# Performance work log

Measured on AMD Instinct MI355X. Metric: run time of the kernel, lower is better.

Reference implementation:

```python
import jax, jax.numpy as jnp
import numpy as np

B, S, D, H = 4, 2048, 1024, 16
HD = D // H

def setup_inputs() -> dict:
    key = jax.random.key(0)
    ks = jax.random.split(key, 11)
    scale = 1.0 / np.sqrt(D)
    return {
        "query": jax.random.normal(ks[0], (B, S, D), jnp.float32),
        "key_": jax.random.normal(ks[1], (B, S, D), jnp.float32),
        "value": jax.random.normal(ks[2], (B, S, D), jnp.float32),
        "wq": jax.random.normal(ks[3], (D, D), jnp.float32) * scale,
        "bq": jnp.zeros((D,), jnp.float32),
        "wk": jax.random.normal(ks[4], (D, D), jnp.float32) * scale,
        "bk": jnp.zeros((D,), jnp.float32),
        "wv": jax.random.normal(ks[5], (D, D), jnp.float32) * scale,
        "bv": jnp.zeros((D,), jnp.float32),
        "wo": jax.random.normal(ks[6], (D, D), jnp.float32) * scale,
        "bo": jnp.zeros((D,), jnp.float32),
    }

def _split_heads(x):
    b, s, _ = x.shape
    return x.reshape(b, s, H, HD).transpose(0, 2, 1, 3)  # [B,H,S,HD]

def reference(query, key_, value, wq, bq, wk, bk, wv, bv, wo, bo):
    q = _split_heads(query @ wq + bq)
    k = _split_heads(key_ @ wk + bk)
    v = _split_heads(value @ wv + bv)
    scores = jnp.einsum('bhqd,bhkd->bhqk', q, k) / jnp.sqrt(jnp.float32(HD))
    attn = jax.nn.softmax(scores, axis=-1)
    ctx = jnp.einsum('bhqk,bhkd->bhqd', attn, v)
    ctx = ctx.transpose(0, 2, 1, 3).reshape(B, S, D)
    return ctx @ wo + bo
```

## Files before the change

kernel.cpp:

```cpp
#include <hip/hip_runtime.h>

typedef _Float16 f16;
typedef _Float16 f16x8 __attribute__((ext_vector_type(8)));
typedef _Float16 f16x4 __attribute__((ext_vector_type(4)));
typedef float    f32x4 __attribute__((ext_vector_type(4)));
typedef float    f32x16 __attribute__((ext_vector_type(16)));

#define MROWS 8192
#define KDIM  1024
#define SEQ   2048
#define HDIM  64
#define QKV_LD 3072

__global__ __launch_bounds__(256) void cast3_k(const float* __restrict__ a,
                                               const float* __restrict__ b,
                                               const float* __restrict__ c,
                                               f16* __restrict__ out) {
  int i = blockIdx.x * 256 + threadIdx.x;
  const float* src = (blockIdx.y == 0) ? a : (blockIdx.y == 1) ? b : c;
  float4 v = ((const float4*)src)[i];
  f16x4 o = { (f16)v.x, (f16)v.y, (f16)v.z, (f16)v.w };
  *(f16x4*)&out[(size_t)blockIdx.y * 8388608 + (size_t)i * 4] = o;
}

__global__ __launch_bounds__(256) void transpose_cast_k(const float* __restrict__ w,
                                                        f16* __restrict__ wt) {
  __shared__ float t[32][33];
  int tx = threadIdx.x, ty = threadIdx.y;
  int bx = blockIdx.x * 32, by = blockIdx.y * 32;
  #pragma unroll
  for (int i = ty; i < 32; i += 8) t[i][tx] = w[(size_t)(by + i) * KDIM + bx + tx];
  __syncthreads();
  #pragma unroll
  for (int i = ty; i < 32; i += 8) wt[(size_t)(bx + i) * KDIM + by + tx] = (f16)t[tx][i];
}

__global__ __launch_bounds__(256) void concat3_k(const float* __restrict__ a,
                                                 const float* __restrict__ b,
                                                 const float* __restrict__ c,
                                                 float* __restrict__ o) {
  int i = blockIdx.x * 256 + threadIdx.x;
  float v;
  if (i < 1024) v = a[i]; else if (i < 2048) v = b[i - 1024]; else v = c[i - 2048];
  o[i] = v;
}

template<bool OUT_F16>
__global__ __launch_bounds__(256) void gemm_k(const f16* __restrict__ A0, size_t aStride,
                                              const f16* __restrict__ Bt,
                                              const float* __restrict__ bias,
                                              void* __restrict__ Cout, int ldc) {
  __shared__ f16 sA[128 * 64];
  __shared__ f16 sB[128 * 64];
  const int tid  = threadIdx.x;
  const int lane = tid & 63;
  const int r    = lane & 15;
  const int q    = lane >> 4;
  const int wave = tid >> 6;
  const int m0 = blockIdx.x * 128;
  const int ng = blockIdx.z * 1024 + blockIdx.y * 128;
  const int wm = (wave >> 1) * 64;
  const int wn = (wave & 1) * 64;
  const f16* A = A0 + (size_t)blockIdx.z * aStride;

  f32x4 acc[4][4];
  #pragma unroll
  for (int i = 0; i < 4; ++i)
    #pragma unroll
    for (int j = 0; j < 4; ++j) acc[i][j] = (f32x4){0.f, 0.f, 0.f, 0.f};

  for (int kt = 0; kt < KDIM; kt += 64) {
    #pragma unroll
    for (int issue = 0; issue < 4; ++issue) {
      int g   = issue * 256 + tid;
      int row = g >> 3;
      int csw = (g & 7) ^ (row & 7);
      const f16* gA = A  + (size_t)(m0 + row) * KDIM + kt + csw * 8;
      const f16* gB = Bt + (size_t)(ng + row) * KDIM + kt + csw * 8;
      int lb = __builtin_amdgcn_readfirstlane((issue * 256 + (tid & ~63)) * 16);
      __builtin_amdgcn_global_load_lds((const __attribute__((address_space(1))) void*)gA,
                                       (__attribute__((address_space(3))) void*)((char*)sA + lb),
                                       16, 0, 0);
      __builtin_amdgcn_global_load_lds((const __attribute__((address_space(1))) void*)gB,
                                       (__attribute__((address_space(3))) void*)((char*)sB + lb),
                                       16, 0, 0);
    }
    __syncthreads();
    #pragma unroll
    for (int kk = 0; kk < 64; kk += 32) {
      f16x8 af[4], bf[4];
      #pragma unroll
      for (int mi = 0; mi < 4; ++mi) {
        int row = wm + mi * 16 + r;
        int cs  = ((kk >> 3) + q) ^ (row & 7);
        af[mi] = *(const f16x8*)&sA[row * 64 + cs * 8];
      }
      #pragma unroll
      for (int ni = 0; ni < 4; ++ni) {
        int row = wn + ni * 16 + r;
        int cs  = ((kk >> 3) + q) ^ (row & 7);
        bf[ni] = *(const f16x8*)&sB[row * 64 + cs * 8];
      }
      #pragma unroll
      for (int mi = 0; mi < 4; ++mi)
        #pragma unroll
        for (int ni = 0; ni < 4; ++ni)
          acc[mi][ni] = __builtin_amdgcn_mfma_f32_16x16x32_f16(af[mi], bf[ni], acc[mi][ni], 0, 0, 0);
    }
    __syncthreads();
  }
  #pragma unroll
  for (int ni = 0; ni < 4; ++ni) {
    int col = ng + wn + ni * 16 + r;
    float bv = bias[col];
    #pragma unroll
    for (int mi = 0; mi < 4; ++mi) {
      int rowb = m0 + wm + mi * 16 + q * 4;
      #pragma unroll
      for (int reg = 0; reg < 4; ++reg) {
        float v = acc[mi][ni][reg] + bv;
        if constexpr (OUT_F16) ((f16*)Cout)[(size_t)(rowb + reg) * ldc + col] = (f16)v;
        else                   ((float*)Cout)[(size_t)(rowb + reg) * ldc + col] = v;
      }
    }
  }
}

__global__ __launch_bounds__(256) void vtrans_k(const f16* __restrict__ qkv,
                                                f16* __restrict__ vt) {
  __shared__ f16 t[64 * 64];
  const int tid = threadIdx.x;
  const int st = blockIdx.x, h = blockIdx.y, b = blockIdx.z;
  const f16* src = qkv + (size_t)(b * SEQ + st * 64) * QKV_LD + 2048 + h * HDIM;
  #pragma unroll
  for (int issue = 0; issue < 2; ++issue) {
    int g = issue * 256 + tid;
    int srow = g >> 3, c = g & 7;
    f16x8 v = *(const f16x8*)(src + (size_t)srow * QKV_LD + c * 8);
    *(f16x8*)&t[srow * 64 + (c ^ (srow & 7)) * 8] = v;
  }
  __syncthreads();
  f16* dst = vt + (size_t)(b * 16 + h) * HDIM * SEQ + st * 64;
  #pragma unroll
  for (int issue = 0; issue < 2; ++issue) {
    int g = issue * 256 + tid;
    int d = g >> 3, c8 = g & 7;
    f16x8 o;
    #pragma unroll
    for (int j = 0; j < 8; ++j) {
      int s = c8 * 8 + j;
      o[j] = t[s * 64 + ((d >> 3) ^ (s & 7)) * 8 + (d & 7)];
    }
    *(f16x8*)(dst + (size_t)d * SEQ + c8 * 8) = o;
  }
}

__global__ __launch_bounds__(256) void attn_k(const f16* __restrict__ qkv,
                                              const f16* __restrict__ vt,
                                              f16* __restrict__ ctx) {
  __shared__ f16 smem[8192];
  f16* sK = smem;
  f16* sV = smem + 4096;
  const int tid  = threadIdx.x;
  const int lane = tid & 63;
  const int wave = tid >> 6;
  const int n    = lane & 31;
  const int q32  = lane >> 5;
  const int x7   = n & 7;
  const int qt = blockIdx.x, h = blockIdx.y, b = blockIdx.z;

  const f16* Qb  = qkv + (size_t)b * SEQ * QKV_LD + h * HDIM;
  const f16* Kb  = Qb + 1024;
  const f16* Vtb = vt + (size_t)(b * 16 + h) * HDIM * SEQ;

  const int qrow = qt * 128 + wave * 32 + n;

  f16x8 qf[4];
  {
    const f16* qp = Qb + (size_t)qrow * QKV_LD + q32 * 8;
    const f16 sc = (f16)(0.125f * 1.44269504f);
    #pragma unroll
    for (int cc = 0; cc < 4; ++cc) qf[cc] = *(const f16x8*)(qp + cc * 16) * sc;
  }

  f32x16 ot[2];
  #pragma unroll
  for (int db = 0; db < 2; ++db)
    #pragma unroll
    for (int i = 0; i < 16; ++i) ot[db][i] = 0.f;
  float ls = 0.f;

  for (int kt = 0; kt < SEQ; kt += 64) {
    #pragma unroll
    for (int issue = 0; issue < 2; ++issue) {
      int g = issue * 256 + tid;
      int row = g >> 3;
      int csw = (g & 7) ^ (row & 7);
      const f16* gK = Kb  + (size_t)(kt + row) * QKV_LD + csw * 8;
      const f16* gV = Vtb + (size_t)row * SEQ + kt + csw * 8;
      int lb = __builtin_amdgcn_readfirstlane((issue * 256 + (tid & ~63)) * 16);
      __builtin_amdgcn_global_load_lds((const __attribute__((address_space(1))) void*)gK,
                                       (__attribute__((address_space(3))) void*)((char*)sK + lb),
                                       16, 0, 0);
      __builtin_amdgcn_global_load_lds((const __attribute__((address_space(1))) void*)gV,
                                       (__attribute__((address_space(3))) void*)((char*)sV + lb),
                                       16, 0, 0);
    }
    __syncthreads();

    f16x4 p[2][4];
    #pragma unroll
    for (int kc = 0; kc < 2; ++kc) {
      f32x16 st;
      #pragma unroll
      for (int i = 0; i < 16; ++i) st[i] = -2.8853901817f;
      #pragma unroll
      for (int cc = 0; cc < 4; ++cc) {
        f16x8 kf = *(const f16x8*)&sK[(kc * 32 + n) * 64 + (((cc * 2 + q32) ^ x7) * 8)];
        st = __builtin_amdgcn_mfma_f32_32x32x16_f16(kf, qf[cc], st, 0, 0, 0);
      }
      #pragma unroll
      for (int g = 0; g < 4; ++g) {
        float e0 = exp2f(st[4 * g + 0]);
        float e1 = exp2f(st[4 * g + 1]);
        float e2 = exp2f(st[4 * g + 2]);
        float e3 = exp2f(st[4 * g + 3]);
        ls += (e0 + e1) + (e2 + e3);
        p[kc][g] = (f16x4){ (f16)e0, (f16)e1, (f16)e2, (f16)e3 };
      }
    }

    #pragma unroll
    for (int db = 0; db < 2; ++db) {
      const f16* vrow = &sV[(db * 32 + n) * 64];
      #pragma unroll
      for (int cc = 0; cc < 4; ++cc) {
        f16x4 vlo = *(const f16x4*)&vrow[(((2 * cc)     ^ x7) * 8) + q32 * 4];
        f16x4 vhi = *(const f16x4*)&vrow[(((2 * cc + 1) ^ x7) * 8) + q32 * 4];
        f16x8 vf = __builtin_shufflevector(vlo, vhi, 0, 1, 2, 3, 4, 5, 6, 7);
        f16x8 pf = __builtin_shufflevector(p[cc >> 1][2 * (cc & 1)],
                                           p[cc >> 1][2 * (cc & 1) + 1],
                                           0, 1, 2, 3, 4, 5, 6, 7);
        ot[db] = __builtin_amdgcn_mfma_f32_32x32x16_f16(vf, pf, ot[db], 0, 0, 0);
      }
    }
    __syncthreads();
  }

  ls += __shfl_xor(ls, 32);
  float inv = 1.0f / ls;

  f16* sO = smem;
  int nl = wave * 32 + n;
  #pragma unroll
  for (int db = 0; db < 2; ++db)
    #pragma unroll
    for (int g = 0; g < 4; ++g) {
      f16x4 o = { (f16)(ot[db][4 * g + 0] * inv), (f16)(ot[db][4 * g + 1] * inv),
                  (f16)(ot[db][4 * g + 2] * inv), (f16)(ot[db][4 * g + 3] * inv) };
      *(f16x4*)&sO[nl * 64 + (((db * 4 + g) ^ (nl & 7)) * 8) + q32 * 4] = o;
    }
  __syncthreads();
  #pragma unroll
  for (int issue = 0; issue < 4; ++issue) {
    int g = issue * 256 + tid;
    int r = g >> 3, sg = g & 7;
    f16x8 v = *(const f16x8*)&sO[r * 64 + ((sg ^ (r & 7)) * 8)];
    *(f16x8*)&ctx[(size_t)(b * SEQ + qt * 128 + r) * KDIM + h * HDIM + sg * 8] = v;
  }
}

extern "C" void kernel_launch(void* const* d_in, const int* in_sizes, int n_in,
                              void* d_out, int out_size, void* d_ws, size_t ws_size,
                              hipStream_t stream) {
  (void)in_sizes; (void)n_in; (void)out_size; (void)ws_size;
  const float* query = (const float*)d_in[0];
  const float* key_  = (const float*)d_in[1];
  const float* value = (const float*)d_in[2];
  const float* wq = (const float*)d_in[3];
  const float* bq = (const float*)d_in[4];
  const float* wk = (const float*)d_in[5];
  const float* bk = (const float*)d_in[6];
  const float* wv = (const float*)d_in[7];
  const float* bv = (const float*)d_in[8];
  const float* wo = (const float*)d_in[9];
  const float* bo = (const float*)d_in[10];
  float* out = (float*)d_out;

  char* ws = (char*)d_ws;
  f16*   X16  = (f16*)(ws);
  f16*   qkvT = (f16*)(ws + 50331648);
  f16*   woT  = (f16*)(ws + 56623104);
  float* b3   = (float*)(ws + 58720256);
  f16*   QKV  = (f16*)(ws + 58736640);
  f16*   ctx  = (f16*)(ws);
  f16*   Vt   = (f16*)(ws + 16777216);

  cast3_k<<<dim3(8192, 3), 256, 0, stream>>>(query, key_, value, X16);
  transpose_cast_k<<<dim3(32, 32), dim3(32, 8), 0, stream>>>(wq, qkvT);
  transpose_cast_k<<<dim3(32, 32), dim3(32, 8), 0, stream>>>(wk, qkvT + 1048576);
  transpose_cast_k<<<dim3(32, 32), dim3(32, 8), 0, stream>>>(wv, qkvT + 2097152);
  transpose_cast_k<<<dim3(32, 32), dim3(32, 8), 0, stream>>>(wo, woT);
  concat3_k<<<12, 256, 0, stream>>>(bq, bk, bv, b3);

  gemm_k<true><<<dim3(64, 8, 3), 256, 0, stream>>>(X16, (size_t)8388608, qkvT, b3, (void*)QKV, QKV_LD);
  vtrans_k<<<dim3(32, 16, 4), 256, 0, stream>>>(QKV, Vt);
  attn_k<<<dim3(16, 16, 4), 256, 0, stream>>>(QKV, Vt, ctx);
  gemm_k<false><<<dim3(64, 8, 1), 256, 0, stream>>>(ctx, (size_t)0, woT, bo, (void*)out, 1024);
}
```

Before: 385.6 us.

## Double-buffer K/V tiles in attention kernel to overlap loads with MFMA

The attention kernel now keeps two LDS buffers for its K/V tiles. It issues the async global-to-LDS loads for the next tile before computing on the current one, so memory latency overlaps with the MFMA and exp work instead of stalling at each barrier. Global pointers are precomputed and advanced each step, and the loop runs two tiles per iteration without unrolling. It also switches to a row XOR (row>>3) LDS swizzle to cut bank conflicts and uses the hardware exp2 builtin. The cost is twice the LDS per block (32KB), which may reduce occupancy.

```diff
diff --git a/kernel.cpp b/kernel.cpp
--- a/kernel.cpp
+++ b/kernel.cpp
@@ -11,6 +11,14 @@
 #define SEQ   2048
 #define HDIM  64
 #define QKV_LD 3072
+
+#if __has_builtin(__builtin_amdgcn_exp2f)
+#define EXP2(x) __builtin_amdgcn_exp2f(x)
+#else
+#define EXP2(x) exp2f(x)
+#endif
+
+__device__ __forceinline__ int swz5(int row) { return (row ^ (row >> 3)) & 7; }
 
 __global__ __launch_bounds__(256) void cast3_k(const float* __restrict__ a,
                                                const float* __restrict__ b,
@@ -158,21 +166,16 @@
 __global__ __launch_bounds__(256) void attn_k(const f16* __restrict__ qkv,
                                               const f16* __restrict__ vt,
                                               f16* __restrict__ ctx) {
-  __shared__ f16 smem[8192];
-  f16* sK = smem;
-  f16* sV = smem + 4096;
+  __shared__ f16 smem[16384];
   const int tid  = threadIdx.x;
   const int lane = tid & 63;
   const int wave = tid >> 6;
   const int n    = lane & 31;
   const int q32  = lane >> 5;
-  const int x7   = n & 7;
   const int qt = blockIdx.x, h = blockIdx.y, b = blockIdx.z;
 
   const f16* Qb  = qkv + (size_t)b * SEQ * QKV_LD + h * HDIM;
-  const f16* Kb  = Qb + 1024;
   const f16* Vtb = vt + (size_t)(b * 16 + h) * HDIM * SEQ;
-
   const int qrow = qt * 128 + wave * 32 + n;
 
   f16x8 qf[4];
@@ -183,6 +186,26 @@
     for (int cc = 0; cc < 4; ++cc) qf[cc] = *(const f16x8*)(qp + cc * 16) * sc;
   }
 
+  const int r0 = tid >> 3, c0 = tid & 7;
+  const f16* gK0 = Qb + 1024 + (size_t)r0 * QKV_LD + (c0 ^ swz5(r0)) * 8;
+  const f16* gK1 = Qb + 1024 + (size_t)(r0 + 32) * QKV_LD + (c0 ^ swz5(r0 + 32)) * 8;
+  const f16* gV0 = Vtb + (size_t)r0 * SEQ + (c0 ^ swz5(r0)) * 8;
+  const f16* gV1 = Vtb + (size_t)(r0 + 32) * SEQ + (c0 ^ swz5(r0 + 32)) * 8;
+  const int lb = __builtin_amdgcn_readfirstlane((tid & ~63) * 16);
+
+  auto stage = [&](int bufbyte) {
+    char* base = (char*)smem + bufbyte + lb;
+    __builtin_amdgcn_global_load_lds((const __attribute__((address_space(1))) void*)gK0,
+                                     (__attribute__((address_space(3))) void*)(base), 16, 0, 0);
+    __builtin_amdgcn_global_load_lds((const __attribute__((address_space(1))) void*)gK1,
+                                     (__attribute__((address_space(3))) void*)(base + 4096), 16, 0, 0);
+    __builtin_amdgcn_global_load_lds((const __attribute__((address_space(1))) void*)gV0,
+                                     (__attribute__((address_space(3))) void*)(base + 8192), 16, 0, 0);
+    __builtin_amdgcn_global_load_lds((const __attribute__((address_space(1))) void*)gV1,
+                                     (__attribute__((address_space(3))) void*)(base + 12288), 16, 0, 0);
+    gK0 += 64 * QKV_LD; gK1 += 64 * QKV_LD; gV0 += 64; gV1 += 64;
+  };
+
   f32x16 ot[2];
   #pragma unroll
   for (int db = 0; db < 2; ++db)
@@ -190,24 +213,9 @@
     for (int i = 0; i < 16; ++i) ot[db][i] = 0.f;
   float ls = 0.f;
 
-  for (int kt = 0; kt < SEQ; kt += 64) {
-    #pragma unroll
-    for (int issue = 0; issue < 2; ++issue) {
-      int g = issue * 256 + tid;
-      int row = g >> 3;
-      int csw = (g & 7) ^ (row & 7);
-      const f16* gK = Kb  + (size_t)(kt + row) * QKV_LD + csw * 8;
-      const f16* gV = Vtb + (size_t)row * SEQ + kt + csw * 8;
-      int lb = __builtin_amdgcn_readfirstlane((issue * 256 + (tid & ~63)) * 16);
-      __builtin_amdgcn_global_load_lds((const __attribute__((address_space(1))) void*)gK,
-                                       (__attribute__((address_space(3))) void*)((char*)sK + lb),
-                                       16, 0, 0);
-      __builtin_amdgcn_global_load_lds((const __attribute__((address_space(1))) void*)gV,
-                                       (__attribute__((address_space(3))) void*)((char*)sV + lb),
-                                       16, 0, 0);
-    }
-    __syncthreads();
-
+  auto compute = [&](int bufe) {
+    const f16* sK = smem + bufe;
+    const f16* sV = smem + bufe + 4096;
     f16x4 p[2][4];
     #pragma unroll
     for (int kc = 0; kc < 2; ++kc) {
@@ -216,27 +224,30 @@
       for (int i = 0; i < 16; ++i) st[i] = -2.8853901817f;
       #pragma unroll
       for (int cc = 0; cc < 4; ++cc) {
-        f16x8 kf = *(const f16x8*)&sK[(kc * 32 + n) * 64 + (((cc * 2 + q32) ^ x7) * 8)];
+        int row = kc * 32 + n;
+        f16x8 kf = *(const f16x8*)&sK[row * 64 + (((cc * 2 + q32) ^ swz5(row)) * 8)];
         st = __builtin_amdgcn_mfma_f32_32x32x16_f16(kf, qf[cc], st, 0, 0, 0);
       }
       #pragma unroll
       for (int g = 0; g < 4; ++g) {
-        float e0 = exp2f(st[4 * g + 0]);
-        float e1 = exp2f(st[4 * g + 1]);
-        float e2 = exp2f(st[4 * g + 2]);
-        float e3 = exp2f(st[4 * g + 3]);
+        float e0 = EXP2(st[4 * g + 0]);
+        float e1 = EXP2(st[4 * g + 1]);
+        float e2 = EXP2(st[4 * g + 2]);
+        float e3 = EXP2(st[4 * g + 3]);
         ls += (e0 + e1) + (e2 + e3);
         p[kc][g] = (f16x4){ (f16)e0, (f16)e1, (f16)e2, (f16)e3 };
       }
     }
-
     #pragma unroll
     for (int db = 0; db < 2; ++db) {
-      const f16* vrow = &sV[(db * 32 + n) * 64];
+      int row = db * 32 + n;
+      int fr = swz5(row);
+      const f16* vrow = &sV[row * 64];
       #pragma unroll
       for (int cc = 0; cc < 4; ++cc) {
-        f16x4 vlo = *(const f16x4*)&vrow[(((2 * cc)     ^ x7) * 8) + q32 * 4];
-        f16x4 vhi = *(const f16x4*)&vrow[(((2 * cc + 1) ^ x7) * 8) + q32 * 4];
+        int hg = (2 * cc) ^ fr;
+        f16x4 vlo = *(const f16x4*)&vrow[hg * 8 + q32 * 4];
+        f16x4 vhi = *(const f16x4*)&vrow[(hg ^ 1) * 8 + q32 * 4];
         f16x8 vf = __builtin_shufflevector(vlo, vhi, 0, 1, 2, 3, 4, 5, 6, 7);
         f16x8 pf = __builtin_shufflevector(p[cc >> 1][2 * (cc & 1)],
                                            p[cc >> 1][2 * (cc & 1) + 1],
@@ -244,7 +255,17 @@
         ot[db] = __builtin_amdgcn_mfma_f32_32x32x16_f16(vf, pf, ot[db], 0, 0, 0);
       }
     }
+  };
+
+  stage(0);
+  #pragma unroll 1
+  for (int it = 0; it < 32; it += 2) {
     __syncthreads();
+    stage(16384);
+    compute(0);
+    __syncthreads();
+    if (it + 2 < 32) stage(0);
+    compute(8192);
   }
 
   ls += __shfl_xor(ls, 32);
@@ -252,21 +273,22 @@
 
   f16* sO = smem;
   int nl = wave * 32 + n;
+  int fo = swz5(nl);
   #pragma unroll
   for (int db = 0; db < 2; ++db)
     #pragma unroll
     for (int g = 0; g < 4; ++g) {
       f16x4 o = { (f16)(ot[db][4 * g + 0] * inv), (f16)(ot[db][4 * g + 1] * inv),
                   (f16)(ot[db][4 * g + 2] * inv), (f16)(ot[db][4 * g + 3] * inv) };
-      *(f16x4*)&sO[nl * 64 + (((db * 4 + g) ^ (nl & 7)) * 8) + q32 * 4] = o;
+      *(f16x4*)&sO[nl * 64 + (((db * 4 + g) ^ fo) * 8) + q32 * 4] = o;
     }
   __syncthreads();
   #pragma unroll
   for (int issue = 0; issue < 4; ++issue) {
     int g = issue * 256 + tid;
-    int r = g >> 3, sg = g & 7;
-    f16x8 v = *(const f16x8*)&sO[r * 64 + ((sg ^ (r & 7)) * 8)];
-    *(f16x8*)&ctx[(size_t)(b * SEQ + qt * 128 + r) * KDIM + h * HDIM + sg * 8] = v;
+    int rr = g >> 3, sg = g & 7;
+    f16x8 v = *(const f16x8*)&sO[rr * 64 + ((sg ^ swz5(rr)) * 8)];
+    *(f16x8*)&ctx[(size_t)(b * SEQ + qt * 128 + rr) * KDIM + h * HDIM + sg * 8] = v;
   }
 }
 
```

New measurement: 362.1 us. 6.1% less time.
